# Performance work log

Measured on AMD Instinct MI355X. Metric: run time of the kernel, lower is better.

## Reference

```python
import jax, jax.numpy as jnp
import numpy as np

N_NODES = 100000
N_EDGES = 1600000
N_PAIRS = 500000
NFEAT = 128
NHID = 128


def _uniform(key, shape, stdv):
    return jax.random.uniform(key, shape, jnp.float32, -stdv, stdv)


def setup_inputs() -> dict:
    key = jax.random.key(0)
    ks = jax.random.split(key, 24)
    inp = {
        'x': jax.random.normal(ks[0], (N_NODES, NFEAT), jnp.float32),
        'edge_row': jax.random.randint(ks[1], (N_EDGES,), 0, N_NODES, jnp.int32),
        'edge_col': jax.random.randint(ks[2], (N_EDGES,), 0, N_NODES, jnp.int32),
        'edge_w': jax.random.uniform(ks[3], (N_EDGES,), jnp.float32),
        'x_idx': jax.random.randint(ks[4], (N_PAIRS,), 0, N_NODES, jnp.int32),
        'y_idx': jax.random.randint(ks[5], (N_PAIRS,), 0, N_NODES, jnp.int32),
    }
    stdv = 1.0 / np.sqrt(NHID)
    # GCN layers: (weight_self, weight_neighbor, bias)
    inp['gc1_ws'] = _uniform(ks[6], (NFEAT, NHID), stdv)
    inp['gc1_wn'] = _uniform(ks[7], (NFEAT, NHID), stdv)
    inp['gc1_b'] = _uniform(ks[8], (NHID,), stdv)
    inp['gc2_ws'] = _uniform(ks[9], (NHID, NHID), stdv)
    inp['gc2_wn'] = _uniform(ks[10], (NHID, NHID), stdv)
    inp['gc2_b'] = _uniform(ks[11], (NHID,), stdv)
    inp['gc3_ws'] = _uniform(ks[12], (NHID, NHID), stdv)
    inp['gc3_wn'] = _uniform(ks[13], (NHID, NHID), stdv)
    inp['gc3_b'] = _uniform(ks[14], (NHID,), stdv)
    # MLP decoder: fc1 (2*nhid -> nhid), fc2 (nhid -> 1)
    s1 = 1.0 / np.sqrt(2 * NHID)
    inp['dec_w1'] = _uniform(ks[15], (2 * NHID, NHID), s1)
    inp['dec_b1'] = _uniform(ks[16], (NHID,), s1)
    s2 = 1.0 / np.sqrt(NHID)
    inp['dec_w2'] = _uniform(ks[17], (NHID, 1), s2)
    inp['dec_b2'] = _uniform(ks[18], (1,), s2)
    return inp


def _gcn(h, ws, wn, b, row, col, w, n_nodes):
    # act_self = h @ W_self ; act_neighbor = adj @ (h @ W_neighbor)
    act_self = h @ ws
    support = h @ wn  # [N, out]
    act_nb = jax.ops.segment_sum(support[col] * w[:, None], row,
                                 num_segments=n_nodes)
    return act_self + act_nb + b


def reference(x, edge_row, edge_col, edge_w, x_idx, y_idx,
              gc1_ws, gc1_wn, gc1_b, gc2_ws, gc2_wn, gc2_b,
              gc3_ws, gc3_wn, gc3_b, dec_w1, dec_b1, dec_w2, dec_b2):
    n = x.shape[0]
    h = jax.nn.relu(_gcn(x, gc1_ws, gc1_wn, gc1_b, edge_row, edge_col, edge_w, n))
    h = jax.nn.relu(_gcn(h, gc2_ws, gc2_wn, gc2_b, edge_row, edge_col, edge_w, n))
    z = _gcn(h, gc3_ws, gc3_wn, gc3_b, edge_row, edge_col, edge_w, n)
    # edge MLP decoder on gathered node pairs
    pair = jnp.concatenate([z[x_idx], z[y_idx]], axis=1)  # [P, 2*nhid]
    hdec = jax.nn.relu(pair @ dec_w1 + dec_b1)
    p = jax.nn.sigmoid(hdec @ dec_w2 + dec_b2)  # [P, 1]
    return (p, z)
```

## Files before the change

kernel.cpp:

```cpp
#include <hip/hip_runtime.h>
#include <hip/hip_bf16.h>

#define N_NODES 100000
#define N_EDGES 1600000
#define N_PAIRS 500000
#define MPAD    100032
#define NF      128

typedef __bf16 bf16x8 __attribute__((ext_vector_type(8)));
typedef float  f32x4  __attribute__((ext_vector_type(4)));
typedef unsigned int   u32;
typedef unsigned short u16;

__device__ inline u16   f2b(float f) { __bf16 b = (__bf16)f; return __builtin_bit_cast(u16, b); }
__device__ inline float b2f(u16 u)   { return (float)__builtin_bit_cast(__bf16, u); }

__global__ void k_convT(const float* __restrict__ src, u16* __restrict__ dst, int K, int N) {
    int i = blockIdx.x * 256 + threadIdx.x;
    if (i >= K * N) return;
    int n = i / K, k = i - n * K;
    dst[i] = f2b(src[k * N + n]);
}

__global__ void k_convX(const float2* __restrict__ x, u32* __restrict__ xb) {
    int i = blockIdx.x * 256 + threadIdx.x;
    if (i >= MPAD * 64) return;
    int node = i >> 6;
    float2 v = make_float2(0.f, 0.f);
    if (node < N_NODES) v = x[i];
    xb[i] = (u32)f2b(v.x) | ((u32)f2b(v.y) << 16);
}

__global__ void k_hist(const int* __restrict__ row, int* __restrict__ deg) {
    int e = blockIdx.x * 256 + threadIdx.x;
    if (e >= N_EDGES) return;
    atomicAdd(&deg[row[e]], 1);
}

__global__ void k_scan1(const int* __restrict__ deg, int* __restrict__ incl, int* __restrict__ bsums) {
    __shared__ int s[1024];
    int t = threadIdx.x;
    int g = blockIdx.x * 1024 + t;
    s[t] = (g < N_NODES) ? deg[g] : 0;
    __syncthreads();
    for (int d = 1; d < 1024; d <<= 1) {
        int add = (t >= d) ? s[t - d] : 0;
        __syncthreads();
        s[t] += add;
        __syncthreads();
    }
    if (g < N_NODES) incl[g] = s[t];
    if (t == 1023) bsums[blockIdx.x] = s[1023];
}

__global__ void k_scan2(int* __restrict__ bsums, int nb) {
    __shared__ int s[128];
    int t = threadIdx.x;
    s[t] = (t < nb) ? bsums[t] : 0;
    __syncthreads();
    for (int d = 1; d < 128; d <<= 1) {
        int add = (t >= d) ? s[t - d] : 0;
        __syncthreads();
        s[t] += add;
        __syncthreads();
    }
    if (t < nb) bsums[t] = (t == 0) ? 0 : s[t - 1];
}

__global__ void k_scan3(const int* __restrict__ incl, const int* __restrict__ bsums,
                        int* __restrict__ rowptr, int* __restrict__ cursor) {
    int g = blockIdx.x * 256 + threadIdx.x;
    if (g == 0) { rowptr[0] = 0; cursor[0] = 0; }
    if (g >= N_NODES) return;
    int v = incl[g] + bsums[g >> 10];
    rowptr[g + 1] = v;
    if (g + 1 < N_NODES) cursor[g + 1] = v;
}

__global__ void k_scatter(const int* __restrict__ row, const int* __restrict__ col,
                          const float* __restrict__ w, int* __restrict__ cursor,
                          int* __restrict__ ccol, float* __restrict__ cw) {
    int e = blockIdx.x * 256 + threadIdx.x;
    if (e >= N_EDGES) return;
    int pos = atomicAdd(&cursor[row[e]], 1);
    ccol[pos] = col[e];
    cw[pos]   = w[e];
}

__global__ void k_gemm_pair(const u16* __restrict__ A, const u16* __restrict__ WsT,
                            const u16* __restrict__ WnT, float* __restrict__ HS,
                            u16* __restrict__ SUP) {
    int wid = threadIdx.x >> 6, lane = threadIdx.x & 63;
    int lr = lane & 15, lg = lane >> 4;
    int m0 = blockIdx.x * 64;
    const u16* WT = (wid < 2) ? WsT : WnT;
    int n0 = (wid & 1) * 64;
    f32x4 acc[4][4] = {};
    for (int ks = 0; ks < 4; ++ks) {
        int k0 = ks * 32 + lg * 8;
        bf16x8 a[4], b[4];
        #pragma unroll
        for (int r = 0; r < 4; ++r)
            a[r] = *reinterpret_cast<const bf16x8*>(A + (size_t)(m0 + r * 16 + lr) * NF + k0);
        #pragma unroll
        for (int c = 0; c < 4; ++c)
            b[c] = *reinterpret_cast<const bf16x8*>(WT + (size_t)(n0 + c * 16 + lr) * NF + k0);
        #pragma unroll
        for (int r = 0; r < 4; ++r)
            #pragma unroll
            for (int c = 0; c < 4; ++c)
                acc[r][c] = __builtin_amdgcn_mfma_f32_16x16x32_bf16(a[r], b[c], acc[r][c], 0, 0, 0);
    }
    #pragma unroll
    for (int r = 0; r < 4; ++r) {
        #pragma unroll
        for (int reg = 0; reg < 4; ++reg) {
            int m = m0 + r * 16 + lg * 4 + reg;
            if (m >= N_NODES) continue;
            #pragma unroll
            for (int c = 0; c < 4; ++c) {
                int col = n0 + c * 16 + lr;
                float v = acc[r][c][reg];
                if (wid < 2) HS[(size_t)m * NF + col] = v;
                else         SUP[(size_t)m * NF + col] = f2b(v);
            }
        }
    }
}

__global__ void k_aggregate(const u32* __restrict__ SUP2, const float2* __restrict__ HS2,
                            const int* __restrict__ rowptr, const int* __restrict__ ccol,
                            const float* __restrict__ cw, const float* __restrict__ bias,
                            u32* __restrict__ Hout, float2* __restrict__ Zout, int relu) {
    int node = blockIdx.x * 4 + (threadIdx.x >> 6);
    int lane = threadIdx.x & 63;
    if (node >= N_NODES) return;
    float a0 = 0.f, a1 = 0.f;
    int e0 = rowptr[node], e1 = rowptr[node + 1];
    for (int e = e0; e < e1; ++e) {
        int c = ccol[e];
        float w = cw[e];
        u32 v = SUP2[(size_t)c * 64 + lane];
        a0 = fmaf(w, b2f((u16)(v & 0xffff)), a0);
        a1 = fmaf(w, b2f((u16)(v >> 16)), a1);
    }
    float2 hsv = HS2[(size_t)node * 64 + lane];
    float o0 = hsv.x + a0 + bias[2 * lane];
    float o1 = hsv.y + a1 + bias[2 * lane + 1];
    if (relu) { o0 = fmaxf(o0, 0.f); o1 = fmaxf(o1, 0.f); }
    Hout[(size_t)node * 64 + lane] = (u32)f2b(o0) | ((u32)f2b(o1) << 16);
    if (Zout) Zout[(size_t)node * 64 + lane] = make_float2(o0, o1);
}

__global__ void k_decoder(const u16* __restrict__ ZB, const int* __restrict__ xidx,
                          const int* __restrict__ yidx, const u16* __restrict__ W1T,
                          const float* __restrict__ b1, const float* __restrict__ w2,
                          const float* __restrict__ b2, float* __restrict__ outp) {
    int wid = threadIdx.x >> 6, lane = threadIdx.x & 63;
    int lr = lane & 15, lg = lane >> 4;
    int p0 = blockIdx.x * 128 + wid * 32;
    int px[2], py[2];
    #pragma unroll
    for (int rt = 0; rt < 2; ++rt) {
        int p = p0 + rt * 16 + lr;
        int pc = (p < N_PAIRS) ? p : 0;
        px[rt] = xidx[pc];
        py[rt] = yidx[pc];
    }
    f32x4 acc[2][8] = {};
    for (int ks = 0; ks < 8; ++ks) {
        int kk = ks * 32 + lg * 8;
        bf16x8 a[2], b[8];
        #pragma unroll
        for (int rt = 0; rt < 2; ++rt) {
            size_t base = (kk < 128) ? ((size_t)px[rt] * NF + kk)
                                     : ((size_t)py[rt] * NF + (kk - 128));
            a[rt] = *reinterpret_cast<const bf16x8*>(ZB + base);
        }
        #pragma unroll
        for (int c = 0; c < 8; ++c)
            b[c] = *reinterpret_cast<const bf16x8*>(W1T + (size_t)(c * 16 + lr) * 256 + kk);
        #pragma unroll
        for (int rt = 0; rt < 2; ++rt)
            #pragma unroll
            for (int c = 0; c < 8; ++c)
                acc[rt][c] = __builtin_amdgcn_mfma_f32_16x16x32_bf16(a[rt], b[c], acc[rt][c], 0, 0, 0);
    }
    float vb1[8], vw2[8];
    #pragma unroll
    for (int c = 0; c < 8; ++c) { int col = c * 16 + lr; vb1[c] = b1[col]; vw2[c] = w2[col]; }
    float vb2 = b2[0];
    #pragma unroll
    for (int rt = 0; rt < 2; ++rt) {
        #pragma unroll
        for (int reg = 0; reg < 4; ++reg) {
            float part = 0.f;
            #pragma unroll
            for (int c = 0; c < 8; ++c) {
                float h = fmaxf(acc[rt][c][reg] + vb1[c], 0.f);
                part = fmaf(h, vw2[c], part);
            }
            #pragma unroll
            for (int m = 1; m < 16; m <<= 1) part += __shfl_xor(part, m, 64);
            int p = p0 + rt * 16 + lg * 4 + reg;
            if (lr == 0 && p < N_PAIRS) outp[p] = 1.f / (1.f + __expf(-(part + vb2)));
        }
    }
}

extern "C" void kernel_launch(void* const* d_in, const int* in_sizes, int n_in,
                              void* d_out, int out_size, void* d_ws, size_t ws_size,
                              hipStream_t stream) {
    const float* x      = (const float*)d_in[0];
    const int* edge_row = (const int*)d_in[1];
    const int* edge_col = (const int*)d_in[2];
    const float* edge_w = (const float*)d_in[3];
    const int* x_idx    = (const int*)d_in[4];
    const int* y_idx    = (const int*)d_in[5];
    const float* gws[3] = {(const float*)d_in[6], (const float*)d_in[9],  (const float*)d_in[12]};
    const float* gwn[3] = {(const float*)d_in[7], (const float*)d_in[10], (const float*)d_in[13]};
    const float* gb[3]  = {(const float*)d_in[8], (const float*)d_in[11], (const float*)d_in[14]};
    const float* dw1 = (const float*)d_in[15];
    const float* db1 = (const float*)d_in[16];
    const float* dw2 = (const float*)d_in[17];
    const float* db2 = (const float*)d_in[18];
    float* out_p = (float*)d_out;
    float* out_z = out_p + N_PAIRS;

    char* base = (char*)d_ws;
    size_t off = 0;
    auto alloc = [&](size_t bytes) -> void* {
        void* p = base + off;
        off = (off + bytes + 255) & ~(size_t)255;
        return p;
    };
    u16* h0  = (u16*)alloc((size_t)MPAD * NF * 2);
    u16* h1  = (u16*)alloc((size_t)MPAD * NF * 2);
    u16* sup = (u16*)alloc((size_t)MPAD * NF * 2);
    float* hs = (float*)alloc((size_t)MPAD * NF * 4);
    u16* wT[6];
    for (int i = 0; i < 6; ++i) wT[i] = (u16*)alloc(128 * 128 * 2);
    u16* w1T  = (u16*)alloc(256 * 128 * 2);
    int* deg    = (int*)alloc(N_NODES * 4);
    int* incl   = (int*)alloc(N_NODES * 4);
    int* bsums  = (int*)alloc(128 * 4);
    int* rowptr = (int*)alloc((N_NODES + 1) * 4);
    int* cursor = (int*)alloc(N_NODES * 4);
    int* ccol   = (int*)alloc(N_EDGES * 4);
    float* cwt  = (float*)alloc(N_EDGES * 4);

    hipMemsetAsync(deg, 0, N_NODES * 4, stream);

    for (int l = 0; l < 3; ++l) {
        k_convT<<<64, 256, 0, stream>>>(gws[l], wT[2 * l],     128, 128);
        k_convT<<<64, 256, 0, stream>>>(gwn[l], wT[2 * l + 1], 128, 128);
    }
    k_convT<<<128, 256, 0, stream>>>(dw1, w1T, 256, 128);
    k_convX<<<(MPAD * 64 + 255) / 256, 256, 0, stream>>>((const float2*)x, (u32*)h0);

    k_hist<<<(N_EDGES + 255) / 256, 256, 0, stream>>>(edge_row, deg);
    k_scan1<<<98, 1024, 0, stream>>>(deg, incl, bsums);
    k_scan2<<<1, 128, 0, stream>>>(bsums, 98);
    k_scan3<<<(N_NODES + 255) / 256, 256, 0, stream>>>(incl, bsums, rowptr, cursor);
    k_scatter<<<(N_EDGES + 255) / 256, 256, 0, stream>>>(edge_row, edge_col, edge_w, cursor, ccol, cwt);

    const int GB = MPAD / 64;
    const int AB = N_NODES / 4;

    k_gemm_pair<<<GB, 256, 0, stream>>>(h0, wT[0], wT[1], hs, sup);
    k_aggregate<<<AB, 256, 0, stream>>>((const u32*)sup, (const float2*)hs, rowptr, ccol, cwt,
                                        gb[0], (u32*)h1, nullptr, 1);
    k_gemm_pair<<<GB, 256, 0, stream>>>(h1, wT[2], wT[3], hs, sup);
    k_aggregate<<<AB, 256, 0, stream>>>((const u32*)sup, (const float2*)hs, rowptr, ccol, cwt,
                                        gb[1], (u32*)h0, nullptr, 1);
    k_gemm_pair<<<GB, 256, 0, stream>>>(h0, wT[4], wT[5], hs, sup);
    k_aggregate<<<AB, 256, 0, stream>>>((const u32*)sup, (const float2*)hs, rowptr, ccol, cwt,
                                        gb[2], (u32*)h1, (float2*)out_z, 0);
    k_decoder<<<(N_PAIRS + 127) / 128, 256, 0, stream>>>(h1, x_idx, y_idx, w1T, db1, dw2, db2, out_p);
}
```

Baseline: 1.115 ms.

## Precompute per-node decoder projections and chunk support layout for aggregation

The decoder's first layer is split algebraically: per-node U = z·W1a + b1 and V = z·W1b are computed once over 100k nodes, replacing a 256-wide GEMM over 500k gathered pairs. A light per-pair kernel then sums U[x] + V[y], applies ReLU, and dots the result with w2. Separately, the support matrix is stored in 16-column chunks and aggregation runs one chunk per block with 8 lanes per node and a 4-way unrolled edge loop. The aim is more edges in flight and better cache locality for the random gathers. U and V are rounded to bf16, and the pair kernel reuses the hs buffer, which adds a little numeric error.

```diff
diff --git a/kernel.cpp b/kernel.cpp
--- a/kernel.cpp
+++ b/kernel.cpp
@@ -89,7 +89,7 @@
 
 __global__ void k_gemm_pair(const u16* __restrict__ A, const u16* __restrict__ WsT,
                             const u16* __restrict__ WnT, float* __restrict__ HS,
-                            u16* __restrict__ SUP) {
+                            u16* __restrict__ SUPc) {
     int wid = threadIdx.x >> 6, lane = threadIdx.x & 63;
     int lr = lane & 15, lg = lane >> 4;
     int m0 = blockIdx.x * 64;
@@ -122,90 +122,132 @@
                 int col = n0 + c * 16 + lr;
                 float v = acc[r][c][reg];
                 if (wid < 2) HS[(size_t)m * NF + col] = v;
-                else         SUP[(size_t)m * NF + col] = f2b(v);
+                else {
+                    int ch = col >> 4, cc = col & 15;
+                    SUPc[((size_t)ch * MPAD + m) * 16 + cc] = f2b(v);
+                }
             }
         }
     }
 }
 
-__global__ void k_aggregate(const u32* __restrict__ SUP2, const float2* __restrict__ HS2,
-                            const int* __restrict__ rowptr, const int* __restrict__ ccol,
-                            const float* __restrict__ cw, const float* __restrict__ bias,
-                            u32* __restrict__ Hout, float2* __restrict__ Zout, int relu) {
-    int node = blockIdx.x * 4 + (threadIdx.x >> 6);
-    int lane = threadIdx.x & 63;
-    if (node >= N_NODES) return;
-    float a0 = 0.f, a1 = 0.f;
-    int e0 = rowptr[node], e1 = rowptr[node + 1];
-    for (int e = e0; e < e1; ++e) {
-        int c = ccol[e];
-        float w = cw[e];
-        u32 v = SUP2[(size_t)c * 64 + lane];
-        a0 = fmaf(w, b2f((u16)(v & 0xffff)), a0);
-        a1 = fmaf(w, b2f((u16)(v >> 16)), a1);
-    }
-    float2 hsv = HS2[(size_t)node * 64 + lane];
-    float o0 = hsv.x + a0 + bias[2 * lane];
-    float o1 = hsv.y + a1 + bias[2 * lane + 1];
-    if (relu) { o0 = fmaxf(o0, 0.f); o1 = fmaxf(o1, 0.f); }
-    Hout[(size_t)node * 64 + lane] = (u32)f2b(o0) | ((u32)f2b(o1) << 16);
-    if (Zout) Zout[(size_t)node * 64 + lane] = make_float2(o0, o1);
-}
-
-__global__ void k_decoder(const u16* __restrict__ ZB, const int* __restrict__ xidx,
-                          const int* __restrict__ yidx, const u16* __restrict__ W1T,
-                          const float* __restrict__ b1, const float* __restrict__ w2,
-                          const float* __restrict__ b2, float* __restrict__ outp) {
+__global__ void k_gemm_uv(const u16* __restrict__ A, const u16* __restrict__ W1aT,
+                          const u16* __restrict__ W1bT, const float* __restrict__ b1,
+                          u16* __restrict__ U, u16* __restrict__ V) {
     int wid = threadIdx.x >> 6, lane = threadIdx.x & 63;
     int lr = lane & 15, lg = lane >> 4;
-    int p0 = blockIdx.x * 128 + wid * 32;
-    int px[2], py[2];
+    int m0 = blockIdx.x * 64;
+    const u16* WT = (wid < 2) ? W1aT : W1bT;
+    u16* OUT = (wid < 2) ? U : V;
+    int addb = (wid < 2) ? 1 : 0;
+    int n0 = (wid & 1) * 64;
+    f32x4 acc[4][4] = {};
+    for (int ks = 0; ks < 4; ++ks) {
+        int k0 = ks * 32 + lg * 8;
+        bf16x8 a[4], b[4];
+        #pragma unroll
+        for (int r = 0; r < 4; ++r)
+            a[r] = *reinterpret_cast<const bf16x8*>(A + (size_t)(m0 + r * 16 + lr) * NF + k0);
+        #pragma unroll
+        for (int c = 0; c < 4; ++c)
+            b[c] = *reinterpret_cast<const bf16x8*>(WT + (size_t)(n0 + c * 16 + lr) * NF + k0);
+        #pragma unroll
+        for (int r = 0; r < 4; ++r)
+            #pragma unroll
+            for (int c = 0; c < 4; ++c)
+                acc[r][c] = __builtin_amdgcn_mfma_f32_16x16x32_bf16(a[r], b[c], acc[r][c], 0, 0, 0);
+    }
     #pragma unroll
-    for (int rt = 0; rt < 2; ++rt) {
-        int p = p0 + rt * 16 + lr;
-        int pc = (p < N_PAIRS) ? p : 0;
-        px[rt] = xidx[pc];
-        py[rt] = yidx[pc];
-    }
-    f32x4 acc[2][8] = {};
-    for (int ks = 0; ks < 8; ++ks) {
-        int kk = ks * 32 + lg * 8;
-        bf16x8 a[2], b[8];
-        #pragma unroll
-        for (int rt = 0; rt < 2; ++rt) {
-            size_t base = (kk < 128) ? ((size_t)px[rt] * NF + kk)
-                                     : ((size_t)py[rt] * NF + (kk - 128));
-            a[rt] = *reinterpret_cast<const bf16x8*>(ZB + base);
+    for (int r = 0; r < 4; ++r) {
+        #pragma unroll
+        for (int reg = 0; reg < 4; ++reg) {
+            int m = m0 + r * 16 + lg * 4 + reg;
+            #pragma unroll
+            for (int c = 0; c < 4; ++c) {
+                int col = n0 + c * 16 + lr;
+                float v = acc[r][c][reg];
+                if (addb) v += b1[col];
+                OUT[(size_t)m * NF + col] = f2b(v);
+            }
         }
-        #pragma unroll
-        for (int c = 0; c < 8; ++c)
-            b[c] = *reinterpret_cast<const bf16x8*>(W1T + (size_t)(c * 16 + lr) * 256 + kk);
-        #pragma unroll
-        for (int rt = 0; rt < 2; ++rt)
-            #pragma unroll
-            for (int c = 0; c < 8; ++c)
-                acc[rt][c] = __builtin_amdgcn_mfma_f32_16x16x32_bf16(a[rt], b[c], acc[rt][c], 0, 0, 0);
-    }
-    float vb1[8], vw2[8];
+    }
+}
+
+__global__ void k_aggregate_c(const u32* __restrict__ SUPc, const float2* __restrict__ HS2,
+                              const int* __restrict__ rowptr, const int* __restrict__ ccol,
+                              const float* __restrict__ cw, const float2* __restrict__ bias2,
+                              u32* __restrict__ Hout, float2* __restrict__ Zout, int relu) {
+    int chunk = blockIdx.x & 7;
+    int nb = blockIdx.x >> 3;
+    int l = threadIdx.x & 63, w = threadIdx.x >> 6;
+    int sub = l >> 3, sl = l & 7;
+    int node = nb * 32 + w * 8 + sub;
+    if (node >= N_NODES) return;
+    const u32* base = SUPc + (size_t)chunk * MPAD * 8;
+    int e0 = rowptr[node], e1 = rowptr[node + 1];
+    float a0 = 0.f, a1 = 0.f;
+    int e = e0;
+    for (; e + 4 <= e1; e += 4) {
+        int c0 = ccol[e], c1 = ccol[e + 1], c2 = ccol[e + 2], c3 = ccol[e + 3];
+        float w0 = cw[e], w1 = cw[e + 1], w2 = cw[e + 2], w3 = cw[e + 3];
+        u32 v0 = base[(size_t)c0 * 8 + sl];
+        u32 v1 = base[(size_t)c1 * 8 + sl];
+        u32 v2 = base[(size_t)c2 * 8 + sl];
+        u32 v3 = base[(size_t)c3 * 8 + sl];
+        a0 = fmaf(w0, b2f((u16)(v0 & 0xffff)), a0); a1 = fmaf(w0, b2f((u16)(v0 >> 16)), a1);
+        a0 = fmaf(w1, b2f((u16)(v1 & 0xffff)), a0); a1 = fmaf(w1, b2f((u16)(v1 >> 16)), a1);
+        a0 = fmaf(w2, b2f((u16)(v2 & 0xffff)), a0); a1 = fmaf(w2, b2f((u16)(v2 >> 16)), a1);
+        a0 = fmaf(w3, b2f((u16)(v3 & 0xffff)), a0); a1 = fmaf(w3, b2f((u16)(v3 >> 16)), a1);
+    }
+    for (; e < e1; ++e) {
+        int c = ccol[e];
+        float wgt = cw[e];
+        u32 v = base[(size_t)c * 8 + sl];
+        a0 = fmaf(wgt, b2f((u16)(v & 0xffff)), a0);
+        a1 = fmaf(wgt, b2f((u16)(v >> 16)), a1);
+    }
+    size_t oidx = (size_t)node * 64 + chunk * 8 + sl;
+    float2 hsv = HS2[oidx];
+    float2 bv  = bias2[chunk * 8 + sl];
+    float o0 = hsv.x + a0 + bv.x;
+    float o1 = hsv.y + a1 + bv.y;
+    if (relu) { o0 = fmaxf(o0, 0.f); o1 = fmaxf(o1, 0.f); }
+    Hout[oidx] = (u32)f2b(o0) | ((u32)f2b(o1) << 16);
+    if (Zout) Zout[oidx] = make_float2(o0, o1);
+}
+
+__global__ void k_pairdec(const u16* __restrict__ U, const u16* __restrict__ V,
+                          const int* __restrict__ xidx, const int* __restrict__ yidx,
+                          const float* __restrict__ w2, const float* __restrict__ b2,
+                          float* __restrict__ outp) {
+    int t = blockIdx.x * 256 + threadIdx.x;
+    int pair = t >> 2;
+    int j = t & 3;
+    if (pair >= N_PAIRS) return;
+    int xi = xidx[pair], yi = yidx[pair];
+    const bf16x8* up = reinterpret_cast<const bf16x8*>(U + (size_t)xi * NF + j * 32);
+    const bf16x8* vp = reinterpret_cast<const bf16x8*>(V + (size_t)yi * NF + j * 32);
+    bf16x8 uu[4], vv[4];
     #pragma unroll
-    for (int c = 0; c < 8; ++c) { int col = c * 16 + lr; vb1[c] = b1[col]; vw2[c] = w2[col]; }
-    float vb2 = b2[0];
+    for (int it = 0; it < 4; ++it) { uu[it] = up[it]; vv[it] = vp[it]; }
+    const float4* w4 = reinterpret_cast<const float4*>(w2 + j * 32);
+    float acc = 0.f;
     #pragma unroll
-    for (int rt = 0; rt < 2; ++rt) {
-        #pragma unroll
-        for (int reg = 0; reg < 4; ++reg) {
-            float part = 0.f;
-            #pragma unroll
-            for (int c = 0; c < 8; ++c) {
-                float h = fmaxf(acc[rt][c][reg] + vb1[c], 0.f);
-                part = fmaf(h, vw2[c], part);
-            }
-            #pragma unroll
-            for (int m = 1; m < 16; m <<= 1) part += __shfl_xor(part, m, 64);
-            int p = p0 + rt * 16 + lg * 4 + reg;
-            if (lr == 0 && p < N_PAIRS) outp[p] = 1.f / (1.f + __expf(-(part + vb2)));
-        }
-    }
+    for (int it = 0; it < 4; ++it) {
+        float4 wa = w4[it * 2], wb = w4[it * 2 + 1];
+        float h;
+        h = fmaxf((float)uu[it][0] + (float)vv[it][0], 0.f); acc = fmaf(h, wa.x, acc);
+        h = fmaxf((float)uu[it][1] + (float)vv[it][1], 0.f); acc = fmaf(h, wa.y, acc);
+        h = fmaxf((float)uu[it][2] + (float)vv[it][2], 0.f); acc = fmaf(h, wa.z, acc);
+        h = fmaxf((float)uu[it][3] + (float)vv[it][3], 0.f); acc = fmaf(h, wa.w, acc);
+        h = fmaxf((float)uu[it][4] + (float)vv[it][4], 0.f); acc = fmaf(h, wb.x, acc);
+        h = fmaxf((float)uu[it][5] + (float)vv[it][5], 0.f); acc = fmaf(h, wb.y, acc);
+        h = fmaxf((float)uu[it][6] + (float)vv[it][6], 0.f); acc = fmaf(h, wb.z, acc);
+        h = fmaxf((float)uu[it][7] + (float)vv[it][7], 0.f); acc = fmaf(h, wb.w, acc);
+    }
+    acc += __shfl_xor(acc, 1, 64);
+    acc += __shfl_xor(acc, 2, 64);
+    if (j == 0) outp[pair] = 1.f / (1.f + __expf(-(acc + b2[0])));
 }
 
 extern "C" void kernel_launch(void* const* d_in, const int* in_sizes, int n_in,
@@ -234,13 +276,14 @@
         off = (off + bytes + 255) & ~(size_t)255;
         return p;
     };
-    u16* h0  = (u16*)alloc((size_t)MPAD * NF * 2);
-    u16* h1  = (u16*)alloc((size_t)MPAD * NF * 2);
-    u16* sup = (u16*)alloc((size_t)MPAD * NF * 2);
+    u16* h0   = (u16*)alloc((size_t)MPAD * NF * 2);
+    u16* h1   = (u16*)alloc((size_t)MPAD * NF * 2);
+    u16* supc = (u16*)alloc((size_t)MPAD * NF * 2);
     float* hs = (float*)alloc((size_t)MPAD * NF * 4);
     u16* wT[6];
     for (int i = 0; i < 6; ++i) wT[i] = (u16*)alloc(128 * 128 * 2);
-    u16* w1T  = (u16*)alloc(256 * 128 * 2);
+    u16* w1aT = (u16*)alloc(128 * 128 * 2);
+    u16* w1bT = (u16*)alloc(128 * 128 * 2);
     int* deg    = (int*)alloc(N_NODES * 4);
     int* incl   = (int*)alloc(N_NODES * 4);
     int* bsums  = (int*)alloc(128 * 4);
@@ -248,6 +291,8 @@
     int* cursor = (int*)alloc(N_NODES * 4);
     int* ccol   = (int*)alloc(N_EDGES * 4);
     float* cwt  = (float*)alloc(N_EDGES * 4);
+    u16* U = (u16*)hs;
+    u16* V = U + (size_t)MPAD * NF;
 
     hipMemsetAsync(deg, 0, N_NODES * 4, stream);
 
@@ -255,7 +300,8 @@
         k_convT<<<64, 256, 0, stream>>>(gws[l], wT[2 * l],     128, 128);
         k_convT<<<64, 256, 0, stream>>>(gwn[l], wT[2 * l + 1], 128, 128);
     }
-    k_convT<<<128, 256, 0, stream>>>(dw1, w1T, 256, 128);
+    k_convT<<<64, 256, 0, stream>>>(dw1,             w1aT, 128, 128);
+    k_convT<<<64, 256, 0, stream>>>(dw1 + 128 * 128, w1bT, 128, 128);
     k_convX<<<(MPAD * 64 + 255) / 256, 256, 0, stream>>>((const float2*)x, (u32*)h0);
 
     k_hist<<<(N_EDGES + 255) / 256, 256, 0, stream>>>(edge_row, deg);
@@ -265,16 +311,17 @@
     k_scatter<<<(N_EDGES + 255) / 256, 256, 0, stream>>>(edge_row, edge_col, edge_w, cursor, ccol, cwt);
 
     const int GB = MPAD / 64;
-    const int AB = N_NODES / 4;
-
-    k_gemm_pair<<<GB, 256, 0, stream>>>(h0, wT[0], wT[1], hs, sup);
-    k_aggregate<<<AB, 256, 0, stream>>>((const u32*)sup, (const float2*)hs, rowptr, ccol, cwt,
-                                        gb[0], (u32*)h1, nullptr, 1);
-    k_gemm_pair<<<GB, 256, 0, stream>>>(h1, wT[2], wT[3], hs, sup);
-    k_aggregate<<<AB, 256, 0, stream>>>((const u32*)sup, (const float2*)hs, rowptr, ccol, cwt,
-                                        gb[1], (u32*)h0, nullptr, 1);
-    k_gemm_pair<<<GB, 256, 0, stream>>>(h0, wT[4], wT[5], hs, sup);
-    k_aggregate<<<AB, 256, 0, stream>>>((const u32*)sup, (const float2*)hs, rowptr, ccol, cwt,
-                                        gb[2], (u32*)h1, (float2*)out_z, 0);
-    k_decoder<<<(N_PAIRS + 127) / 128, 256, 0, stream>>>(h1, x_idx, y_idx, w1T, db1, dw2, db2, out_p);
-}
+    const int AB = 8 * ((N_NODES + 31) / 32);
+
+    k_gemm_pair<<<GB, 256, 0, stream>>>(h0, wT[0], wT[1], hs, supc);
+    k_aggregate_c<<<AB, 256, 0, stream>>>((const u32*)supc, (const float2*)hs, rowptr, ccol, cwt,
+                                          (const float2*)gb[0], (u32*)h1, nullptr, 1);
+    k_gemm_pair<<<GB, 256, 0, stream>>>(h1, wT[2], wT[3], hs, supc);
+    k_aggregate_c<<<AB, 256, 0, stream>>>((const u32*)supc, (const float2*)hs, rowptr, ccol, cwt,
+                                          (const float2*)gb[1], (u32*)h0, nullptr, 1);
+    k_gemm_pair<<<GB, 256, 0, stream>>>(h0, wT[4], wT[5], hs, supc);
+    k_aggregate_c<<<AB, 256, 0, stream>>>((const u32*)supc, (const float2*)hs, rowptr, ccol, cwt,
+                                          (const float2*)gb[2], (u32*)h1, (float2*)out_z, 0);
+    k_gemm_uv<<<GB, 256, 0, stream>>>(h1, w1aT, w1bT, db1, U, V);
+    k_pairdec<<<(N_PAIRS * 4 + 255) / 256, 256, 0, stream>>>(U, V, x_idx, y_idx, dw2, db2, out_p);
+}
```

Result: faster. 905.0 us (-18.8%).
